# Performance work log

Hardware: AMD Instinct MI355X
Metric: run time of the kernel (lower is better)

## Reference

```python
import jax, jax.numpy as jnp
import numpy as np

S = 8192      # total packed tokens
H = 1152      # hidden size
NH = 16       # heads
HD = 72       # head dim
NSEG = 8      # number of packed (equal-length) sequences
L = S // NSEG # tokens per sequence
SCALE = HD ** -0.5


def setup_inputs() -> dict:
    key = jax.random.key(0)
    ks = jax.random.split(key, 4)
    hidden_states = jax.random.normal(ks[0], (1, S, H), jnp.float32)
    # Real rotary cos/sin per token position within each sequence.
    inv_freq = 1.0 / (10000.0 ** (np.arange(0, HD, 2, dtype=np.float64) / HD))
    freqs = np.outer(np.arange(L, dtype=np.float64), inv_freq)  # [L, HD/2]
    emb = np.concatenate([freqs, freqs], axis=-1)               # [L, HD]
    cos = jnp.asarray(np.tile(np.cos(emb), (NSEG, 1)), jnp.float32)  # [S, HD]
    sin = jnp.asarray(np.tile(np.sin(emb), (NSEG, 1)), jnp.float32)
    Wqkv = jax.random.normal(ks[1], (H, 3 * H), jnp.float32) * (H ** -0.5)
    bqkv = jnp.zeros((3 * H,), jnp.float32)
    Wout = jax.random.normal(ks[2], (H, H), jnp.float32) * (H ** -0.5)
    bout = jnp.zeros((H,), jnp.float32)
    cu_seqlens = jnp.arange(NSEG + 1, dtype=jnp.int32) * L
    return dict(hidden_states=hidden_states, cos=cos, sin=sin,
                Wqkv=Wqkv, bqkv=bqkv, Wout=Wout, bout=bout,
                cu_seqlens=cu_seqlens)


def _rotate_half(x):
    return jnp.concatenate([-x[..., HD // 2:], x[..., :HD // 2]], axis=-1)


def reference(hidden_states, cos, sin, Wqkv, bqkv, Wout, bout, cu_seqlens):
    # QKV projection (fused)
    qkv = hidden_states @ Wqkv + bqkv                 # [1, S, 3H]
    q, k, v = jnp.split(qkv, [H, 2 * H], axis=-1)
    q = q.reshape(1, S, NH, HD)
    k = k.reshape(1, S, NH, HD)
    v = v.reshape(1, S, NH, HD)
    # Inline RoPE on q/k (cos/sin broadcast over heads)
    c = cos[None, :, None, :]
    s = sin[None, :, None, :]
    q = q * c + _rotate_half(q) * s
    k = k * c + _rotate_half(k) * s
    # Varlen (block-diagonal) non-causal attention: equal-length segments
    q = q.reshape(NSEG, L, NH, HD)
    k = k.reshape(NSEG, L, NH, HD)
    v = v.reshape(NSEG, L, NH, HD)
    scores = jnp.einsum('nqhd,nkhd->nhqk', q, k) * SCALE  # [NSEG, NH, L, L]
    probs = jax.nn.softmax(scores, axis=-1)
    ctx = jnp.einsum('nhqk,nkhd->nqhd', probs, v)         # [NSEG, L, NH, HD]
    ctx = ctx.reshape(1, S, H)
    # Output projection
    return ctx @ Wout + bout
```

## Files before the change

### kernel.cpp

```cpp
#include <hip/hip_runtime.h>
#include <hip/hip_fp16.h>
#include <cstdint>

typedef _Float16 half8 __attribute__((ext_vector_type(8)));
typedef _Float16 half4 __attribute__((ext_vector_type(4)));
typedef float floatx4 __attribute__((ext_vector_type(4)));

#define S_TOT 8192
#define H_DIM 1152
#define NHEAD 16
#define HD 72
#define HDP 96
#define NSEG 8
#define SEGL 1024
#define QSCALE 0.17002324631230988f

__device__ __forceinline__ void gld_lds16(const void* g, void* l) {
  __builtin_amdgcn_global_load_lds((const __attribute__((address_space(1))) void*)g,
                                   (__attribute__((address_space(3))) void*)l, 16, 0, 0);
}

__global__ void cast_f32_f16(const float* __restrict__ in, _Float16* __restrict__ out, int n) {
  int i = (blockIdx.x * 256 + threadIdx.x) * 4;
  if (i < n) {
    float4 v = *(const float4*)(in + i);
    half4 o = { (_Float16)v.x, (_Float16)v.y, (_Float16)v.z, (_Float16)v.w };
    *(half4*)(out + i) = o;
  }
}

__global__ void transpose_cast(const float* __restrict__ W, _Float16* __restrict__ Wt,
                               int R, int C) {
  __shared__ float tile[32][33];
  int tx = threadIdx.x, ty = threadIdx.y;
  int bx = blockIdx.x, by = blockIdx.y;
#pragma unroll
  for (int i = 0; i < 4; ++i)
    tile[ty + i * 8][tx] = W[(size_t)(by * 32 + ty + i * 8) * C + bx * 32 + tx];
  __syncthreads();
#pragma unroll
  for (int i = 0; i < 4; ++i)
    Wt[(size_t)(bx * 32 + ty + i * 8) * R + by * 32 + tx] = (_Float16)tile[tx][ty + i * 8];
}

template <bool OUT_HALF>
__global__ __launch_bounds__(256) void gemm_bt(
    const _Float16* __restrict__ A, const _Float16* __restrict__ Bt,
    const float* __restrict__ bias, float* __restrict__ Cf, _Float16* __restrict__ Ch,
    int M, int N, int K) {
  __shared__ _Float16 As[128 * 32];
  __shared__ _Float16 Bs[128 * 32];
  const int tid = threadIdx.x;
  const int lane = tid & 63, w = tid >> 6;
  const int quad = lane >> 4, l16 = lane & 15;
  const int wm = w >> 1, wn = w & 1;
  const int m0 = blockIdx.y * 128, n0 = blockIdx.x * 128;

  floatx4 acc[4][4] = {};

  for (int kt = 0; kt < K; kt += 32) {
    __syncthreads();
#pragma unroll
    for (int i = 0; i < 2; ++i) {
      int off = tid * 16 + i * 4096;
      int row = off >> 6, colb = off & 63;
      gld_lds16((const char*)(A + (size_t)(m0 + row) * K + kt) + colb, (char*)As + off);
      gld_lds16((const char*)(Bt + (size_t)(n0 + row) * K + kt) + colb, (char*)Bs + off);
    }
    __syncthreads();
    half8 af[4], bf[4];
#pragma unroll
    for (int im = 0; im < 4; ++im)
      af[im] = *(const half8*)&As[(wm * 64 + im * 16 + l16) * 32 + quad * 8];
#pragma unroll
    for (int in = 0; in < 4; ++in)
      bf[in] = *(const half8*)&Bs[(wn * 64 + in * 16 + l16) * 32 + quad * 8];
#pragma unroll
    for (int im = 0; im < 4; ++im)
#pragma unroll
      for (int in = 0; in < 4; ++in)
        acc[im][in] = __builtin_amdgcn_mfma_f32_16x16x32_f16(af[im], bf[in], acc[im][in], 0, 0, 0);
  }
#pragma unroll
  for (int im = 0; im < 4; ++im) {
    int m = m0 + wm * 64 + im * 16 + quad * 4;
#pragma unroll
    for (int in = 0; in < 4; ++in) {
      int n = n0 + wn * 64 + in * 16 + l16;
      float b = bias[n];
#pragma unroll
      for (int r = 0; r < 4; ++r) {
        float v = acc[im][in][r] + b;
        if (OUT_HALF) Ch[(size_t)(m + r) * N + n] = (_Float16)v;
        else          Cf[(size_t)(m + r) * N + n] = v;
      }
    }
  }
}

__global__ void rope_scatter(const _Float16* __restrict__ QKV,
                             const float* __restrict__ cosb,
                             const float* __restrict__ sinb,
                             _Float16* __restrict__ Qo, _Float16* __restrict__ Ko,
                             _Float16* __restrict__ Vo) {
  int t = blockIdx.x * 256 + threadIdx.x;
  int s = t >> 4, h = t & 15;
  int n = s >> 10, l = s & 1023;
  const _Float16* q = QKV + (size_t)s * 3456 + h * HD;
  const _Float16* k = q + H_DIM;
  const _Float16* v = q + 2 * H_DIM;
  const float* cs = cosb + (size_t)s * HD;
  const float* sn = sinb + (size_t)s * HD;
  size_t oo = (((size_t)(n * NHEAD + h)) * SEGL + l) * HDP;
  half8 z = {};
  {
    _Float16 qr[72], qo[72];
#pragma unroll
    for (int i = 0; i < 9; ++i) *(half8*)&qr[8 * i] = *(const half8*)(q + 8 * i);
#pragma unroll
    for (int d = 0; d < 36; ++d) {
      float c0 = cs[d], s0 = sn[d], c1 = cs[d + 36], s1 = sn[d + 36];
      float a = (float)qr[d], b = (float)qr[d + 36];
      qo[d]      = (_Float16)((a * c0 - b * s0) * QSCALE);
      qo[d + 36] = (_Float16)((b * c1 + a * s1) * QSCALE);
    }
#pragma unroll
    for (int i = 0; i < 9; ++i) *(half8*)(Qo + oo + 8 * i) = *(half8*)&qo[8 * i];
#pragma unroll
    for (int i = 9; i < 12; ++i) *(half8*)(Qo + oo + 8 * i) = z;
  }
  {
    _Float16 kr[72], ko[72];
#pragma unroll
    for (int i = 0; i < 9; ++i) *(half8*)&kr[8 * i] = *(const half8*)(k + 8 * i);
#pragma unroll
    for (int d = 0; d < 36; ++d) {
      float c0 = cs[d], s0 = sn[d], c1 = cs[d + 36], s1 = sn[d + 36];
      float a = (float)kr[d], b = (float)kr[d + 36];
      ko[d]      = (_Float16)(a * c0 - b * s0);
      ko[d + 36] = (_Float16)(b * c1 + a * s1);
    }
#pragma unroll
    for (int i = 0; i < 9; ++i) *(half8*)(Ko + oo + 8 * i) = *(half8*)&ko[8 * i];
#pragma unroll
    for (int i = 9; i < 12; ++i) *(half8*)(Ko + oo + 8 * i) = z;
  }
#pragma unroll
  for (int i = 0; i < 9; ++i) *(half8*)(Vo + oo + 8 * i) = *(const half8*)(v + 8 * i);
#pragma unroll
  for (int i = 9; i < 12; ++i) *(half8*)(Vo + oo + 8 * i) = z;
}

__global__ __launch_bounds__(256) void attn_kernel(
    const _Float16* __restrict__ Qb, const _Float16* __restrict__ Kb,
    const _Float16* __restrict__ Vb, _Float16* __restrict__ Ctx) {
  __shared__ _Float16 Kt[64 * 96];
  __shared__ _Float16 Vt[80 * 72];
  __shared__ _Float16 Ps[4 * 32 * 72];
  const int tid = threadIdx.x;
  const int lane = tid & 63, w = tid >> 6;
  const int quad = lane >> 4, l16 = lane & 15;
  const int qb = blockIdx.x, h = blockIdx.y, n = blockIdx.z;
  const size_t headoff = ((size_t)(n * NHEAD + h)) * SEGL * HDP;
  const _Float16* Qg = Qb + headoff;
  const _Float16* Kg = Kb + headoff;
  const _Float16* Vg = Vb + headoff;

  half8 qf[2][3];
#pragma unroll
  for (int qg = 0; qg < 2; ++qg) {
    int row = qb * 128 + w * 32 + qg * 16 + l16;
#pragma unroll
    for (int kc = 0; kc < 3; ++kc)
      qf[qg][kc] = *(const half8*)(Qg + (size_t)row * HDP + kc * 32 + quad * 8);
  }
  float m_s[2] = {-1e30f, -1e30f}, l_s[2] = {0.f, 0.f};
  floatx4 o_acc[2][5] = {};

  for (int kb = 0; kb < SEGL / 64; ++kb) {
    __syncthreads();
    {
      const char* base = (const char*)(Kg + (size_t)kb * 64 * HDP);
#pragma unroll
      for (int i = 0; i < 3; ++i) {
        int off = tid * 16 + i * 4096;
        gld_lds16(base + off, (char*)Kt + off);
      }
    }
#pragma unroll
    for (int i = 0; i < 3; ++i) {
      int dg = w * 3 + i;
      if (dg < 10) {
        half8 vv = *(const half8*)(Vg + (size_t)(kb * 64 + lane) * HDP + dg * 8);
#pragma unroll
        for (int j = 0; j < 8; ++j) Vt[(dg * 8 + j) * 72 + lane] = vv[j];
      }
    }
    __syncthreads();
    floatx4 sa[2][4] = {};
#pragma unroll
    for (int nt = 0; nt < 4; ++nt) {
#pragma unroll
      for (int kc = 0; kc < 3; ++kc) {
        half8 kf = *(const half8*)&Kt[(nt * 16 + l16) * 96 + kc * 32 + quad * 8];
        sa[0][nt] = __builtin_amdgcn_mfma_f32_16x16x32_f16(kf, qf[0][kc], sa[0][nt], 0, 0, 0);
        sa[1][nt] = __builtin_amdgcn_mfma_f32_16x16x32_f16(kf, qf[1][kc], sa[1][nt], 0, 0, 0);
      }
    }
#pragma unroll
    for (int qg = 0; qg < 2; ++qg) {
      float mx = -1e30f;
#pragma unroll
      for (int nt = 0; nt < 4; ++nt)
#pragma unroll
        for (int r = 0; r < 4; ++r) mx = fmaxf(mx, sa[qg][nt][r]);
      mx = fmaxf(mx, __shfl_xor(mx, 16, 64));
      mx = fmaxf(mx, __shfl_xor(mx, 32, 64));
      float mnew = fmaxf(m_s[qg], mx);
      float alpha = exp2f(m_s[qg] - mnew);
      float sum = 0.f;
#pragma unroll
      for (int nt = 0; nt < 4; ++nt)
#pragma unroll
        for (int r = 0; r < 4; ++r) {
          float p = exp2f(sa[qg][nt][r] - mnew);
          sa[qg][nt][r] = p;
          sum += p;
        }
      sum += __shfl_xor(sum, 16, 64);
      sum += __shfl_xor(sum, 32, 64);
      l_s[qg] = l_s[qg] * alpha + sum;
      m_s[qg] = mnew;
#pragma unroll
      for (int t = 0; t < 5; ++t) o_acc[qg][t] *= alpha;
      int prow = (w * 32 + qg * 16 + l16) * 72;
#pragma unroll
      for (int nt = 0; nt < 4; ++nt) {
        half4 ph = { (_Float16)sa[qg][nt][0], (_Float16)sa[qg][nt][1],
                     (_Float16)sa[qg][nt][2], (_Float16)sa[qg][nt][3] };
        *(half4*)&Ps[prow + nt * 16 + quad * 4] = ph;
      }
    }
#pragma unroll
    for (int kc2 = 0; kc2 < 2; ++kc2) {
      half8 pb0 = *(const half8*)&Ps[(w * 32 + l16) * 72 + kc2 * 32 + quad * 8];
      half8 pb1 = *(const half8*)&Ps[(w * 32 + 16 + l16) * 72 + kc2 * 32 + quad * 8];
#pragma unroll
      for (int t = 0; t < 5; ++t) {
        half8 vf = *(const half8*)&Vt[(t * 16 + l16) * 72 + kc2 * 32 + quad * 8];
        o_acc[0][t] = __builtin_amdgcn_mfma_f32_16x16x32_f16(vf, pb0, o_acc[0][t], 0, 0, 0);
        o_acc[1][t] = __builtin_amdgcn_mfma_f32_16x16x32_f16(vf, pb1, o_acc[1][t], 0, 0, 0);
      }
    }
  }
#pragma unroll
  for (int qg = 0; qg < 2; ++qg) {
    float rl = 1.0f / l_s[qg];
    size_t s2 = (size_t)n * SEGL + qb * 128 + w * 32 + qg * 16 + l16;
#pragma unroll
    for (int t = 0; t < 5; ++t) {
      int d0 = t * 16 + quad * 4;
      if (d0 < HD) {
        half4 hv = { (_Float16)(o_acc[qg][t][0] * rl), (_Float16)(o_acc[qg][t][1] * rl),
                     (_Float16)(o_acc[qg][t][2] * rl), (_Float16)(o_acc[qg][t][3] * rl) };
        *(half4*)&Ctx[s2 * H_DIM + h * HD + d0] = hv;
      }
    }
  }
}

extern "C" void kernel_launch(void* const* d_in, const int* in_sizes, int n_in,
                              void* d_out, int out_size, void* d_ws, size_t ws_size,
                              hipStream_t stream) {
  const float* X    = (const float*)d_in[0];
  const float* cosb = (const float*)d_in[1];
  const float* sinb = (const float*)d_in[2];
  const float* Wqkv = (const float*)d_in[3];
  const float* bqkv = (const float*)d_in[4];
  const float* Wout = (const float*)d_in[5];
  const float* bout = (const float*)d_in[6];
  float* out = (float*)d_out;
  char* ws = (char*)d_ws;

  _Float16* Xb   = (_Float16*)(ws);
  _Float16* Wqt  = (_Float16*)(ws + 18874368);
  _Float16* Wot  = (_Float16*)(ws + 26836992);
  _Float16* QKVb = (_Float16*)(ws + 29491200);
  _Float16* Qb   = (_Float16*)(ws + 86114304);
  _Float16* Kb   = (_Float16*)(ws + 111280128);
  _Float16* Vb   = (_Float16*)(ws + 136445952);
  _Float16* Ctx  = (_Float16*)(ws + 161611776);

  cast_f32_f16<<<9216, 256, 0, stream>>>(X, Xb, S_TOT * H_DIM);
  transpose_cast<<<dim3(108, 36), dim3(32, 8), 0, stream>>>(Wqkv, Wqt, H_DIM, 3 * H_DIM);
  transpose_cast<<<dim3(36, 36), dim3(32, 8), 0, stream>>>(Wout, Wot, H_DIM, H_DIM);
  gemm_bt<true><<<dim3(27, 64), 256, 0, stream>>>(Xb, Wqt, bqkv, nullptr, QKVb,
                                                  S_TOT, 3 * H_DIM, H_DIM);
  rope_scatter<<<512, 256, 0, stream>>>(QKVb, cosb, sinb, Qb, Kb, Vb);
  attn_kernel<<<dim3(8, 16, 8), 256, 0, stream>>>(Qb, Kb, Vb, Ctx);
  gemm_bt<false><<<dim3(9, 64), 256, 0, stream>>>(Ctx, Wot, bout, out, nullptr,
                                                  S_TOT, H_DIM, H_DIM);
}
```

Before: 432.8 us.

## Pre-transpose V per key tile and pad K stride to avoid LDS bank conflicts

Adds a separate transpose_v kernel that writes V into per-64-key tiles already in the [d][key] layout the attention PV MFMA expects. The attention loop can then fill its V tile with direct global-to-LDS async loads instead of scattering it element by element inside the hot loop. K rows are stored with a 104-element stride, meant to cut LDS bank conflicts on the K fragment reads. The cost is one extra kernel launch and an extra pass over V, and Ctx now reuses the Xb buffer.

Result: no change. 436.2 us (+0.8%).

```diff
diff --git a/kernel.cpp b/kernel.cpp
--- a/kernel.cpp
+++ b/kernel.cpp
@@ -10,10 +10,12 @@
 #define H_DIM 1152
 #define NHEAD 16
 #define HD 72
-#define HDP 96
+#define QSTR 96
+#define KSTR 104
 #define NSEG 8
 #define SEGL 1024
 #define QSCALE 0.17002324631230988f
+#define VT_TILE 5760
 
 __device__ __forceinline__ void gld_lds16(const void* g, void* l) {
   __builtin_amdgcn_global_load_lds((const __attribute__((address_space(1))) void*)g,
@@ -48,8 +50,8 @@
     const _Float16* __restrict__ A, const _Float16* __restrict__ Bt,
     const float* __restrict__ bias, float* __restrict__ Cf, _Float16* __restrict__ Ch,
     int M, int N, int K) {
-  __shared__ _Float16 As[128 * 32];
-  __shared__ _Float16 Bs[128 * 32];
+  __shared__ __align__(16) _Float16 As[128 * 32];
+  __shared__ __align__(16) _Float16 Bs[128 * 32];
   const int tid = threadIdx.x;
   const int lane = tid & 63, w = tid >> 6;
   const int quad = lane >> 4, l16 = lane & 15;
@@ -101,70 +103,91 @@
 __global__ void rope_scatter(const _Float16* __restrict__ QKV,
                              const float* __restrict__ cosb,
                              const float* __restrict__ sinb,
-                             _Float16* __restrict__ Qo, _Float16* __restrict__ Ko,
-                             _Float16* __restrict__ Vo) {
+                             _Float16* __restrict__ Qo, _Float16* __restrict__ Ko) {
   int t = blockIdx.x * 256 + threadIdx.x;
   int s = t >> 4, h = t & 15;
   int n = s >> 10, l = s & 1023;
   const _Float16* q = QKV + (size_t)s * 3456 + h * HD;
   const _Float16* k = q + H_DIM;
-  const _Float16* v = q + 2 * H_DIM;
   const float* cs = cosb + (size_t)s * HD;
   const float* sn = sinb + (size_t)s * HD;
-  size_t oo = (((size_t)(n * NHEAD + h)) * SEGL + l) * HDP;
+  size_t row = ((size_t)(n * NHEAD + h)) * SEGL + l;
+  size_t qo = row * QSTR, ko = row * KSTR;
   half8 z = {};
   {
-    _Float16 qr[72], qo[72];
+    _Float16 qr[72], qv[72];
 #pragma unroll
     for (int i = 0; i < 9; ++i) *(half8*)&qr[8 * i] = *(const half8*)(q + 8 * i);
 #pragma unroll
     for (int d = 0; d < 36; ++d) {
       float c0 = cs[d], s0 = sn[d], c1 = cs[d + 36], s1 = sn[d + 36];
       float a = (float)qr[d], b = (float)qr[d + 36];
-      qo[d]      = (_Float16)((a * c0 - b * s0) * QSCALE);
-      qo[d + 36] = (_Float16)((b * c1 + a * s1) * QSCALE);
-    }
-#pragma unroll
-    for (int i = 0; i < 9; ++i) *(half8*)(Qo + oo + 8 * i) = *(half8*)&qo[8 * i];
-#pragma unroll
-    for (int i = 9; i < 12; ++i) *(half8*)(Qo + oo + 8 * i) = z;
+      qv[d]      = (_Float16)((a * c0 - b * s0) * QSCALE);
+      qv[d + 36] = (_Float16)((b * c1 + a * s1) * QSCALE);
+    }
+#pragma unroll
+    for (int i = 0; i < 9; ++i) *(half8*)(Qo + qo + 8 * i) = *(half8*)&qv[8 * i];
+#pragma unroll
+    for (int i = 9; i < 12; ++i) *(half8*)(Qo + qo + 8 * i) = z;
   }
   {
-    _Float16 kr[72], ko[72];
+    _Float16 kr[72], kv[72];
 #pragma unroll
     for (int i = 0; i < 9; ++i) *(half8*)&kr[8 * i] = *(const half8*)(k + 8 * i);
 #pragma unroll
     for (int d = 0; d < 36; ++d) {
       float c0 = cs[d], s0 = sn[d], c1 = cs[d + 36], s1 = sn[d + 36];
       float a = (float)kr[d], b = (float)kr[d + 36];
-      ko[d]      = (_Float16)(a * c0 - b * s0);
-      ko[d + 36] = (_Float16)(b * c1 + a * s1);
-    }
-#pragma unroll
-    for (int i = 0; i < 9; ++i) *(half8*)(Ko + oo + 8 * i) = *(half8*)&ko[8 * i];
-#pragma unroll
-    for (int i = 9; i < 12; ++i) *(half8*)(Ko + oo + 8 * i) = z;
-  }
-#pragma unroll
-  for (int i = 0; i < 9; ++i) *(half8*)(Vo + oo + 8 * i) = *(const half8*)(v + 8 * i);
-#pragma unroll
-  for (int i = 9; i < 12; ++i) *(half8*)(Vo + oo + 8 * i) = z;
+      kv[d]      = (_Float16)(a * c0 - b * s0);
+      kv[d + 36] = (_Float16)(b * c1 + a * s1);
+    }
+#pragma unroll
+    for (int i = 0; i < 9; ++i) *(half8*)(Ko + ko + 8 * i) = *(half8*)&kv[8 * i];
+#pragma unroll
+    for (int i = 9; i < 12; ++i) *(half8*)(Ko + ko + 8 * i) = z;
+  }
+}
+
+__global__ __launch_bounds__(256) void transpose_v(const _Float16* __restrict__ QKV,
+                                                   _Float16* __restrict__ Vt) {
+  __shared__ __align__(16) _Float16 Vs[64 * 88];
+  const int tid = threadIdx.x;
+  const int kb = blockIdx.x, h = blockIdx.y, n = blockIdx.z;
+  const int s0 = n * SEGL + kb * 64;
+  const _Float16* src = QKV + (size_t)s0 * 3456 + 2 * H_DIM + h * HD;
+  for (int idx = tid; idx < 576; idx += 256) {
+    int key = idx / 9, c = idx - key * 9;
+    *(half8*)&Vs[key * 88 + c * 8] = *(const half8*)(src + (size_t)key * 3456 + c * 8);
+  }
+  __syncthreads();
+  _Float16* dst = Vt + (((size_t)(n * NHEAD + h)) * 16 + kb) * VT_TILE;
+  for (int idx = tid; idx < 720; idx += 256) {
+    int d = idx / 9, c = idx - d * 9;
+    half8 v;
+    if (d < HD) {
+#pragma unroll
+      for (int j = 0; j < 8; ++j) v[j] = Vs[(c * 8 + j) * 88 + d];
+    } else {
+      v = half8{};
+    }
+    *(half8*)(dst + d * 72 + c * 8) = v;
+  }
 }
 
 __global__ __launch_bounds__(256) void attn_kernel(
     const _Float16* __restrict__ Qb, const _Float16* __restrict__ Kb,
-    const _Float16* __restrict__ Vb, _Float16* __restrict__ Ctx) {
-  __shared__ _Float16 Kt[64 * 96];
-  __shared__ _Float16 Vt[80 * 72];
-  __shared__ _Float16 Ps[4 * 32 * 72];
+    const _Float16* __restrict__ Vtb, _Float16* __restrict__ Ctx) {
+  __shared__ __align__(16) _Float16 Kt[64 * KSTR];
+  __shared__ __align__(16) _Float16 Vt[80 * 72];
+  __shared__ __align__(16) _Float16 Ps[4 * 32 * 72];
   const int tid = threadIdx.x;
   const int lane = tid & 63, w = tid >> 6;
   const int quad = lane >> 4, l16 = lane & 15;
   const int qb = blockIdx.x, h = blockIdx.y, n = blockIdx.z;
-  const size_t headoff = ((size_t)(n * NHEAD + h)) * SEGL * HDP;
-  const _Float16* Qg = Qb + headoff;
-  const _Float16* Kg = Kb + headoff;
-  const _Float16* Vg = Vb + headoff;
+  const size_t hseg = (size_t)(n * NHEAD + h);
+  const _Float16* Qg = Qb + hseg * SEGL * QSTR;
+  const _Float16* Kg = Kb + hseg * SEGL * KSTR;
+  const _Float16* Vg = Vtb + hseg * 16 * VT_TILE;
 
   half8 qf[2][3];
 #pragma unroll
@@ -172,7 +195,7 @@
     int row = qb * 128 + w * 32 + qg * 16 + l16;
 #pragma unroll
     for (int kc = 0; kc < 3; ++kc)
-      qf[qg][kc] = *(const half8*)(Qg + (size_t)row * HDP + kc * 32 + quad * 8);
+      qf[qg][kc] = *(const half8*)(Qg + (size_t)row * QSTR + kc * 32 + quad * 8);
   }
   float m_s[2] = {-1e30f, -1e30f}, l_s[2] = {0.f, 0.f};
   floatx4 o_acc[2][5] = {};
@@ -180,21 +203,20 @@
   for (int kb = 0; kb < SEGL / 64; ++kb) {
     __syncthreads();
     {
-      const char* base = (const char*)(Kg + (size_t)kb * 64 * HDP);
-#pragma unroll
-      for (int i = 0; i < 3; ++i) {
-        int off = tid * 16 + i * 4096;
-        gld_lds16(base + off, (char*)Kt + off);
-      }
-    }
-#pragma unroll
-    for (int i = 0; i < 3; ++i) {
-      int dg = w * 3 + i;
-      if (dg < 10) {
-        half8 vv = *(const half8*)(Vg + (size_t)(kb * 64 + lane) * HDP + dg * 8);
-#pragma unroll
-        for (int j = 0; j < 8; ++j) Vt[(dg * 8 + j) * 72 + lane] = vv[j];
-      }
+      const char* base = (const char*)(Kg + (size_t)kb * 64 * KSTR);
+#pragma unroll
+      for (int i = 0; i < 3; ++i)
+        gld_lds16(base + tid * 16 + i * 4096, (char*)Kt + tid * 16 + i * 4096);
+      if (tid < 64)
+        gld_lds16(base + 12288 + tid * 16, (char*)Kt + 12288 + tid * 16);
+    }
+    {
+      const char* base = (const char*)(Vg + (size_t)kb * VT_TILE);
+#pragma unroll
+      for (int i = 0; i < 2; ++i)
+        gld_lds16(base + tid * 16 + i * 4096, (char*)Vt + tid * 16 + i * 4096);
+      if (tid < 208)
+        gld_lds16(base + 8192 + tid * 16, (char*)Vt + 8192 + tid * 16);
     }
     __syncthreads();
     floatx4 sa[2][4] = {};
@@ -202,7 +224,7 @@
     for (int nt = 0; nt < 4; ++nt) {
 #pragma unroll
       for (int kc = 0; kc < 3; ++kc) {
-        half8 kf = *(const half8*)&Kt[(nt * 16 + l16) * 96 + kc * 32 + quad * 8];
+        half8 kf = *(const half8*)&Kt[(nt * 16 + l16) * KSTR + kc * 32 + quad * 8];
         sa[0][nt] = __builtin_amdgcn_mfma_f32_16x16x32_f16(kf, qf[0][kc], sa[0][nt], 0, 0, 0);
         sa[1][nt] = __builtin_amdgcn_mfma_f32_16x16x32_f16(kf, qf[1][kc], sa[1][nt], 0, 0, 0);
       }
@@ -288,16 +310,17 @@
   _Float16* QKVb = (_Float16*)(ws + 29491200);
   _Float16* Qb   = (_Float16*)(ws + 86114304);
   _Float16* Kb   = (_Float16*)(ws + 111280128);
-  _Float16* Vb   = (_Float16*)(ws + 136445952);
-  _Float16* Ctx  = (_Float16*)(ws + 161611776);
+  _Float16* Vtb  = (_Float16*)(ws + 138543104);
+  _Float16* Ctx  = Xb;
 
   cast_f32_f16<<<9216, 256, 0, stream>>>(X, Xb, S_TOT * H_DIM);
   transpose_cast<<<dim3(108, 36), dim3(32, 8), 0, stream>>>(Wqkv, Wqt, H_DIM, 3 * H_DIM);
   transpose_cast<<<dim3(36, 36), dim3(32, 8), 0, stream>>>(Wout, Wot, H_DIM, H_DIM);
   gemm_bt<true><<<dim3(27, 64), 256, 0, stream>>>(Xb, Wqt, bqkv, nullptr, QKVb,
                                                   S_TOT, 3 * H_DIM, H_DIM);
-  rope_scatter<<<512, 256, 0, stream>>>(QKVb, cosb, sinb, Qb, Kb, Vb);
-  attn_kernel<<<dim3(8, 16, 8), 256, 0, stream>>>(Qb, Kb, Vb, Ctx);
+  rope_scatter<<<512, 256, 0, stream>>>(QKVb, cosb, sinb, Qb, Kb);
+  transpose_v<<<dim3(16, 16, 8), 256, 0, stream>>>(QKVb, Vtb);
+  attn_kernel<<<dim3(8, 16, 8), 256, 0, stream>>>(Qb, Kb, Vtb, Ctx);
   gemm_bt<false><<<dim3(9, 64), 256, 0, stream>>>(Ctx, Wot, bout, out, nullptr,
                                                   S_TOT, H_DIM, H_DIM);
 }
```
